# Kernel tuning notes

Measured on AMD Instinct MI355X. Metric: run time of the kernel, lower is better.

Reference implementation:

```python
import jax, jax.numpy as jnp
import numpy as np

B, S, N, H, V = 8, 512, 32, 256, 100001
NEG = -1e9
SLOPE = 0.2  # LeakyReLU negative slope


def setup_inputs() -> dict:
    key = jax.random.key(0)
    k1, k2, k3, k4, k5 = jax.random.split(key, 5)
    node_ids = jax.random.randint(k1, (B, S), 0, V)
    neighs = jax.random.randint(k2, (B, S, N), 0, V)
    mask = jax.random.randint(k3, (B, S, N, 1), 0, 2).astype(jnp.int32)
    emb_table = jax.random.normal(k4, (V, H), dtype=jnp.float32) * 0.02
    a_w = jax.random.normal(k5, (2 * H, 1), dtype=jnp.float32) * (1.0 / np.sqrt(2 * H))
    a_b = jnp.zeros((1,), dtype=jnp.float32)
    return {"node_ids": node_ids, "neighs": neighs, "mask": mask,
            "emb_table": emb_table, "a_w": a_w, "a_b": a_b}


def reference(node_ids, neighs, mask, emb_table, a_w, a_b):
    # Gather embeddings
    src = emb_table[node_ids][:, :, None, :]          # [B,S,1,H]
    nbr = emb_table[neighs]                           # [B,S,N,H]
    neigh_embs = jnp.concatenate([src, nbr], axis=2)  # [B,S,N+1,H] (self + neighbors)
    # Concat src with each candidate -> [B,S,N+1,2H]
    src_rep = jnp.broadcast_to(src, neigh_embs.shape)
    embs = jnp.concatenate([src_rep, neigh_embs], axis=-1)
    # Tiny linear (2H -> 1) + LeakyReLU(0.2)
    z = embs @ a_w + a_b                              # [B,S,N+1,1]
    att = jnp.where(z > 0, z, SLOPE * z)
    # Mask neighbor slots (self at index 0 is never masked)
    att = att.at[:, :, 1:].add(mask.astype(att.dtype) * NEG)
    w = jax.nn.softmax(att, axis=2)                   # [B,S,N+1,1]
    # Weighted aggregate: w^T @ neigh_embs
    out = jnp.sum(w * neigh_embs, axis=2)             # [B,S,H]
    return out
```

## Files before the change

kernel.cpp:

```cpp
#include <hip/hip_runtime.h>


constexpr int H  = 256;
constexpr int NN = 32;
constexpr int C  = NN + 1;
constexpr float SLOPE = 0.2f;
constexpr float NEGV  = -1e9f;

__device__ __forceinline__ float wave_sum(float v) {
#pragma unroll
  for (int off = 32; off > 0; off >>= 1)
    v += __shfl_xor(v, off, 64);
  return v;
}

__global__ __launch_bounds__(256, 2) void gat_kernel(
    const int*   __restrict__ node_ids,
    const int*   __restrict__ neighs,
    const int*   __restrict__ mask,
    const float* __restrict__ emb,
    const float* __restrict__ a_w,
    const float* __restrict__ a_b,
    float*       __restrict__ out,
    int npos)
{
  const int wid  = (blockIdx.x * blockDim.x + threadIdx.x) >> 6;
  const int lane = threadIdx.x & 63;
  if (wid >= npos) return;
  const int pos = wid;
  const int l4  = lane << 2;

  const float4 aw1 = *(const float4*)(a_w + l4);
  const float4 aw2 = *(const float4*)(a_w + H + l4);
  const float  ab  = a_b[0];

  int idx[C];
  idx[0] = node_ids[pos];
#pragma unroll
  for (int n = 0; n < NN; ++n) idx[n + 1] = neighs[pos * NN + n];

  float4 e[C];
#pragma unroll
  for (int c = 0; c < C; ++c)
    e[c] = *(const float4*)(emb + (size_t)idx[c] * H + l4);

  const float zsrc = e[0].x * aw1.x + e[0].y * aw1.y +
                     e[0].z * aw1.z + e[0].w * aw1.w;

  float att[C];
#pragma unroll
  for (int c = 0; c < C; ++c) {
    float p = zsrc + e[c].x * aw2.x + e[c].y * aw2.y +
                     e[c].z * aw2.z + e[c].w * aw2.w;
    att[c] = wave_sum(p);
  }

#pragma unroll
  for (int c = 0; c < C; ++c) {
    float z = att[c] + ab;
    float a = (z > 0.f) ? z : SLOPE * z;
    if (c > 0) a += mask[pos * NN + (c - 1)] ? NEGV : 0.f;
    att[c] = a;
  }

  float m = att[0];
#pragma unroll
  for (int c = 1; c < C; ++c) m = fmaxf(m, att[c]);
  float s = 0.f;
#pragma unroll
  for (int c = 0; c < C; ++c) { att[c] = __expf(att[c] - m); s += att[c]; }
  const float inv = 1.f / s;

  float4 acc = {0.f, 0.f, 0.f, 0.f};
#pragma unroll
  for (int c = 0; c < C; ++c) {
    const float w = att[c] * inv;
    acc.x += w * e[c].x;
    acc.y += w * e[c].y;
    acc.z += w * e[c].z;
    acc.w += w * e[c].w;
  }
  *(float4*)(out + (size_t)pos * H + l4) = acc;
}

extern "C" void kernel_launch(void* const* d_in, const int* in_sizes, int n_in,
                              void* d_out, int out_size, void* d_ws, size_t ws_size,
                              hipStream_t stream) {
  const int*   node_ids = (const int*)d_in[0];
  const int*   neighs   = (const int*)d_in[1];
  const int*   mask     = (const int*)d_in[2];
  const float* emb      = (const float*)d_in[3];
  const float* a_w      = (const float*)d_in[4];
  const float* a_b      = (const float*)d_in[5];
  float*       out      = (float*)d_out;

  const int npos = in_sizes[0];
  const int waves_per_block = 256 / 64;
  const int grid = (npos + waves_per_block - 1) / waves_per_block;

  gat_kernel<<<grid, 256, 0, stream>>>(node_ids, neighs, mask, emb, a_w, a_b,
                                       out, npos);
}
```

Baseline: 165.0 us.

## Stream neighbor rows through prefetch ring with online softmax aggregation

Replaces holding all 33 gathered embedding rows in registers with an 8-deep prefetch ring and an online (running max) softmax that accumulates the weighted sum as rows arrive. Indices and mask are loaded once, one per lane, and broadcast via shuffles instead of every lane loading all of them, and launch bounds are raised to allow more waves per SIMD. The aim is to cut register pressure and raise occupancy to hide gather latency. The cost is extra exp and rescale work per row and less memory-level parallelism per wave, since only 8 loads are in flight instead of 33.

```diff
diff --git a/kernel.cpp b/kernel.cpp
--- a/kernel.cpp
+++ b/kernel.cpp
@@ -1,9 +1,11 @@
 #include <hip/hip_runtime.h>
+#include <math.h>
 
 
 constexpr int H  = 256;
 constexpr int NN = 32;
 constexpr int C  = NN + 1;
+constexpr int PF = 8;
 constexpr float SLOPE = 0.2f;
 constexpr float NEGV  = -1e9f;
 
@@ -14,7 +16,7 @@
   return v;
 }
 
-__global__ __launch_bounds__(256, 2) void gat_kernel(
+__global__ __launch_bounds__(256, 4) void gat_kernel(
     const int*   __restrict__ node_ids,
     const int*   __restrict__ neighs,
     const int*   __restrict__ mask,
@@ -27,60 +29,64 @@
   const int wid  = (blockIdx.x * blockDim.x + threadIdx.x) >> 6;
   const int lane = threadIdx.x & 63;
   if (wid >= npos) return;
-  const int pos = wid;
-  const int l4  = lane << 2;
+  const int l4 = lane << 2;
 
   const float4 aw1 = *(const float4*)(a_w + l4);
   const float4 aw2 = *(const float4*)(a_w + H + l4);
   const float  ab  = a_b[0];
 
-  int idx[C];
-  idx[0] = node_ids[pos];
+  int   my_idx  = 0;
+  float my_madd = 0.f;
+  if (lane == 0) {
+    my_idx = node_ids[wid];
+  } else if (lane <= NN) {
+    my_idx  = neighs[wid * NN + lane - 1];
+    my_madd = mask[wid * NN + lane - 1] ? NEGV : 0.f;
+  }
+
+  const float4* __restrict__ embv = (const float4*)emb;
+
+  auto row_lane = [&](int c) -> float4 {
+    int ic = __builtin_amdgcn_readfirstlane(__shfl(my_idx, c, 64));
+    return embv[(size_t)ic * (H / 4) + lane];
+  };
+
+  float4 buf[PF];
 #pragma unroll
-  for (int n = 0; n < NN; ++n) idx[n + 1] = neighs[pos * NN + n];
+  for (int i = 0; i < PF; ++i) buf[i] = row_lane(i);
 
-  float4 e[C];
-#pragma unroll
-  for (int c = 0; c < C; ++c)
-    e[c] = *(const float4*)(emb + (size_t)idx[c] * H + l4);
-
-  const float zsrc = e[0].x * aw1.x + e[0].y * aw1.y +
-                     e[0].z * aw1.z + e[0].w * aw1.w;
-
-  float att[C];
-#pragma unroll
-  for (int c = 0; c < C; ++c) {
-    float p = zsrc + e[c].x * aw2.x + e[c].y * aw2.y +
-                     e[c].z * aw2.z + e[c].w * aw2.w;
-    att[c] = wave_sum(p);
-  }
+  float  m = -1e30f, s = 0.f;
+  float  zsrc = 0.f;
+  float4 acc = {0.f, 0.f, 0.f, 0.f};
 
 #pragma unroll
   for (int c = 0; c < C; ++c) {
-    float z = att[c] + ab;
+    const float4 cur = buf[c & (PF - 1)];
+    if (c + PF < C) buf[c & (PF - 1)] = row_lane(c + PF);
+
+    float p = cur.x * aw2.x + cur.y * aw2.y + cur.z * aw2.z + cur.w * aw2.w;
+    if (c == 0) {
+      float ps = cur.x * aw1.x + cur.y * aw1.y + cur.z * aw1.z + cur.w * aw1.w;
+      zsrc = wave_sum(ps);
+    }
+    float z = zsrc + wave_sum(p) + ab;
     float a = (z > 0.f) ? z : SLOPE * z;
-    if (c > 0) a += mask[pos * NN + (c - 1)] ? NEGV : 0.f;
-    att[c] = a;
+    a += __shfl(my_madd, c, 64);
+
+    const float mnew  = fmaxf(m, a);
+    const float scale = __expf(m - mnew);
+    const float pr    = __expf(a - mnew);
+    s = s * scale + pr;
+    acc.x = acc.x * scale + pr * cur.x;
+    acc.y = acc.y * scale + pr * cur.y;
+    acc.z = acc.z * scale + pr * cur.z;
+    acc.w = acc.w * scale + pr * cur.w;
+    m = mnew;
   }
 
-  float m = att[0];
-#pragma unroll
-  for (int c = 1; c < C; ++c) m = fmaxf(m, att[c]);
-  float s = 0.f;
-#pragma unroll
-  for (int c = 0; c < C; ++c) { att[c] = __expf(att[c] - m); s += att[c]; }
   const float inv = 1.f / s;
-
-  float4 acc = {0.f, 0.f, 0.f, 0.f};
-#pragma unroll
-  for (int c = 0; c < C; ++c) {
-    const float w = att[c] * inv;
-    acc.x += w * e[c].x;
-    acc.y += w * e[c].y;
-    acc.z += w * e[c].z;
-    acc.w += w * e[c].w;
-  }
-  *(float4*)(out + (size_t)pos * H + l4) = acc;
+  float4 o = {acc.x * inv, acc.y * inv, acc.z * inv, acc.w * inv};
+  *(float4*)(out + (size_t)wid * H + l4) = o;
 }
 
 extern "C" void kernel_launch(void* const* d_in, const int* in_sizes, int n_in,
```

New measurement: 158.4 us. 1.04x faster.

## Skip masked neighbors and refetch embeddings to cut registers and raise occupancy

Applied to the files above, without the earlier changes.

Each lane now loads one neighbor index and its mask bit, and the wave reads them back as scalars with readlane. Masked neighbors, whose softmax weight is exactly zero, are skipped for the gather, the dot products, the reductions and the aggregation. Embedding rows are no longer kept in 33 float4 registers. They are gathered once for the attention scores and again for the weighted sum, which allows a launch bound of 6 blocks instead of 2. This cuts gather traffic by about the masked fraction, at the cost of a second pass of loads that must hit in cache to stay cheap.

```diff
diff --git a/kernel.cpp b/kernel.cpp
--- a/kernel.cpp
+++ b/kernel.cpp
@@ -1,20 +1,13 @@
 #include <hip/hip_runtime.h>
+#include <math.h>
 
 
 constexpr int H  = 256;
 constexpr int NN = 32;
 constexpr int C  = NN + 1;
 constexpr float SLOPE = 0.2f;
-constexpr float NEGV  = -1e9f;
 
-__device__ __forceinline__ float wave_sum(float v) {
-#pragma unroll
-  for (int off = 32; off > 0; off >>= 1)
-    v += __shfl_xor(v, off, 64);
-  return v;
-}
-
-__global__ __launch_bounds__(256, 2) void gat_kernel(
+__global__ __launch_bounds__(256, 6) void gat_kernel(
     const int*   __restrict__ node_ids,
     const int*   __restrict__ neighs,
     const int*   __restrict__ mask,
@@ -27,60 +20,92 @@
   const int wid  = (blockIdx.x * blockDim.x + threadIdx.x) >> 6;
   const int lane = threadIdx.x & 63;
   if (wid >= npos) return;
-  const int pos = wid;
-  const int l4  = lane << 2;
+  const int l4 = lane << 2;
 
   const float4 aw1 = *(const float4*)(a_w + l4);
   const float4 aw2 = *(const float4*)(a_w + H + l4);
   const float  ab  = a_b[0];
 
-  int idx[C];
-  idx[0] = node_ids[pos];
+  int my_idx = 0, my_mact = 1;
+  if (lane == 0) {
+    my_idx  = node_ids[wid];
+    my_mact = 0;
+  } else if (lane <= NN) {
+    my_idx  = neighs[wid * NN + lane - 1];
+    my_mact = mask[wid * NN + lane - 1];
+  }
+
+  const float4* __restrict__ embv = (const float4*)emb;
+
+  float red[C];
+  float zp;
+  {
+    const int i0 = __builtin_amdgcn_readlane(my_idx, 0);
+    const float4 e0 = embv[(size_t)i0 * (H / 4) + lane];
+    zp     = e0.x * aw1.x + e0.y * aw1.y + e0.z * aw1.z + e0.w * aw1.w;
+    red[0] = e0.x * aw2.x + e0.y * aw2.y + e0.z * aw2.z + e0.w * aw2.w;
+  }
 #pragma unroll
-  for (int n = 0; n < NN; ++n) idx[n + 1] = neighs[pos * NN + n];
-
-  float4 e[C];
-#pragma unroll
-  for (int c = 0; c < C; ++c)
-    e[c] = *(const float4*)(emb + (size_t)idx[c] * H + l4);
-
-  const float zsrc = e[0].x * aw1.x + e[0].y * aw1.y +
-                     e[0].z * aw1.z + e[0].w * aw1.w;
-
-  float att[C];
-#pragma unroll
-  for (int c = 0; c < C; ++c) {
-    float p = zsrc + e[c].x * aw2.x + e[c].y * aw2.y +
-                     e[c].z * aw2.z + e[c].w * aw2.w;
-    att[c] = wave_sum(p);
+  for (int c = 1; c < C; ++c) {
+    const int mc = __builtin_amdgcn_readlane(my_mact, c);
+    if (mc == 0) {
+      const int ic = __builtin_amdgcn_readlane(my_idx, c);
+      const float4 e = embv[(size_t)ic * (H / 4) + lane];
+      red[c] = e.x * aw2.x + e.y * aw2.y + e.z * aw2.z + e.w * aw2.w;
+    } else {
+      red[c] = 0.f;
+    }
   }
 
 #pragma unroll
+  for (int off = 32; off > 0; off >>= 1)
+    zp += __shfl_xor(zp, off, 64);
+#pragma unroll
   for (int c = 0; c < C; ++c) {
-    float z = att[c] + ab;
-    float a = (z > 0.f) ? z : SLOPE * z;
-    if (c > 0) a += mask[pos * NN + (c - 1)] ? NEGV : 0.f;
-    att[c] = a;
+    const int mc = __builtin_amdgcn_readlane(my_mact, c);
+    if (mc == 0) {
+#pragma unroll
+      for (int off = 32; off > 0; off >>= 1)
+        red[c] += __shfl_xor(red[c], off, 64);
+    }
   }
 
-  float m = att[0];
+  float m = -1e30f;
 #pragma unroll
-  for (int c = 1; c < C; ++c) m = fmaxf(m, att[c]);
+  for (int c = 0; c < C; ++c) {
+    const int mc = __builtin_amdgcn_readlane(my_mact, c);
+    if (mc == 0) {
+      const float z = zp + red[c] + ab;
+      red[c] = (z > 0.f) ? z : SLOPE * z;
+      m = fmaxf(m, red[c]);
+    }
+  }
   float s = 0.f;
 #pragma unroll
-  for (int c = 0; c < C; ++c) { att[c] = __expf(att[c] - m); s += att[c]; }
+  for (int c = 0; c < C; ++c) {
+    const int mc = __builtin_amdgcn_readlane(my_mact, c);
+    if (mc == 0) {
+      red[c] = __expf(red[c] - m);
+      s += red[c];
+    }
+  }
   const float inv = 1.f / s;
 
   float4 acc = {0.f, 0.f, 0.f, 0.f};
 #pragma unroll
   for (int c = 0; c < C; ++c) {
-    const float w = att[c] * inv;
-    acc.x += w * e[c].x;
-    acc.y += w * e[c].y;
-    acc.z += w * e[c].z;
-    acc.w += w * e[c].w;
+    const int mc = __builtin_amdgcn_readlane(my_mact, c);
+    if (mc == 0) {
+      const int ic = __builtin_amdgcn_readlane(my_idx, c);
+      const float4 e = embv[(size_t)ic * (H / 4) + lane];
+      const float w = red[c] * inv;
+      acc.x += w * e.x;
+      acc.y += w * e.y;
+      acc.z += w * e.z;
+      acc.w += w * e.w;
+    }
   }
-  *(float4*)(out + (size_t)pos * H + l4) = acc;
+  *(float4*)(out + (size_t)wid * H + l4) = acc;
 }
 
 extern "C" void kernel_launch(void* const* d_in, const int* in_sizes, int n_in,
```

Measured after the change: 168.1 us. About the same (+1.9%).
